# Kernel tuning notes

Measured on AMD Instinct MI355X. Metric: run time of the kernel, lower is better.

## Reference

```python
import jax, jax.numpy as jnp
import numpy as np
from jax import lax

B, T, IN, H = 32, 512, 512, 512
NUM_LAYERS, NUM_DIR = 2, 2


def _lstm_layer(inputs, Wx, Wh, bx, bh, reverse):
    """inputs: [T,B,D]; Wx: [4H,D]; Wh: [4H,H]; bx,bh: [4H]. Returns (hs [T,B,H], hT, cT)."""
    Tn, Bn, _ = inputs.shape
    Hn = Wh.shape[1]
    # Precompute input-to-hidden projections for all timesteps (one big GEMM).
    xg = jnp.einsum('tbd,gd->tbg', inputs, Wx) + bx + bh  # [T,B,4H]
    if reverse:
        xg = xg[::-1]

    def step(carry, xg_t):
        h, c = carry
        g = xg_t + h @ Wh.T  # [B,4H]
        i, f, gg, o = jnp.split(g, 4, axis=-1)  # PyTorch LSTM gate order i,f,g,o
        i = jax.nn.sigmoid(i)
        f = jax.nn.sigmoid(f)
        gg = jnp.tanh(gg)
        o = jax.nn.sigmoid(o)
        c = f * c + i * gg
        h = o * jnp.tanh(c)
        return (h, c), h

    h0 = jnp.zeros((Bn, Hn), dtype=inputs.dtype)
    (hT, cT), hs = lax.scan(step, (h0, h0), xg)
    if reverse:
        hs = hs[::-1]
    return hs, hT, cT


def setup_inputs() -> dict:
    key = jax.random.key(0)
    ks = jax.random.split(key, 20)
    std = 1.0 / np.sqrt(H)
    u = lambda k, shp: jax.random.uniform(k, shp, jnp.float32, -std, std)
    inp = {
        'x': jax.random.normal(ks[0], (B, T, IN), jnp.float32),
        # layer 0: input dim IN, stacked over 2 directions
        'Wx_l0': u(ks[1], (NUM_DIR, 4 * H, IN)),
        'Wh_l0': u(ks[2], (NUM_DIR, 4 * H, H)),
        'bx_l0': u(ks[3], (NUM_DIR, 4 * H)),
        'bh_l0': u(ks[4], (NUM_DIR, 4 * H)),
        # layer 1: input dim 2H (bidirectional concat)
        'Wx_l1': u(ks[5], (NUM_DIR, 4 * H, NUM_DIR * H)),
        'Wh_l1': u(ks[6], (NUM_DIR, 4 * H, H)),
        'bx_l1': u(ks[7], (NUM_DIR, 4 * H)),
        'bh_l1': u(ks[8], (NUM_DIR, 4 * H)),
    }
    return inp


def reference(x, Wx_l0, Wh_l0, bx_l0, bh_l0, Wx_l1, Wh_l1, bx_l1, bh_l1):
    layer_params = [(Wx_l0, Wh_l0, bx_l0, bh_l0), (Wx_l1, Wh_l1, bx_l1, bh_l1)]
    inputs = jnp.transpose(x, (1, 0, 2))  # [T,B,IN] (batch_first -> time-major)
    h_list, c_list = [], []
    for layer in range(NUM_LAYERS):
        Wx, Wh, bx, bh = layer_params[layer]
        dir_outs = []
        for d in range(NUM_DIR):
            hs, hT, cT = _lstm_layer(inputs, Wx[d], Wh[d], bx[d], bh[d], reverse=(d == 1))
            dir_outs.append(hs)
            h_list.append(hT)
            c_list.append(cT)
        inputs = jnp.concatenate(dir_outs, axis=-1)  # [T,B,2H] (dropout=0.0)
    output = jnp.transpose(inputs, (1, 0, 2))  # [B,T,2H]
    h_n = jnp.stack(h_list)  # [num_layers*num_dir, B, H]
    c_n = jnp.stack(c_list)
    return output, h_n, c_n
```

## Files before the change

### kernel.cpp

```cpp
#include <hip/hip_runtime.h>

typedef _Float16 f16;
typedef _Float16 f16x2 __attribute__((ext_vector_type(2)));
typedef _Float16 f16x4 __attribute__((ext_vector_type(4)));
typedef _Float16 f16x8 __attribute__((ext_vector_type(8)));
typedef float f32x4 __attribute__((ext_vector_type(4)));

#define AS1 __attribute__((address_space(1)))
#define AS3 __attribute__((address_space(3)))

static __device__ __forceinline__ float sigf(float x) { return 1.f / (1.f + __expf(-x)); }
static __device__ __forceinline__ float tanh_f(float x) { return 2.f / (1.f + __expf(-2.f * x)) - 1.f; }

__global__ void f2h_kernel(const float* __restrict__ in, f16* __restrict__ out, int n4) {
  const int i = blockIdx.x * blockDim.x + threadIdx.x;
  if (i >= n4) return;
  const float4 v = ((const float4*)in)[i];
  f16x4 o;
  o[0] = (f16)v.x; o[1] = (f16)v.y; o[2] = (f16)v.z; o[3] = (f16)v.w;
  ((f16x4*)out)[i] = o;
}

__global__ void bias_kernel(const float* __restrict__ a, const float* __restrict__ b,
                            float* __restrict__ o, int n) {
  const int i = blockIdx.x * blockDim.x + threadIdx.x;
  if (i < n) o[i] = a[i] + b[i];
}

__global__ __launch_bounds__(256) void gemm_xg(const f16* __restrict__ A,
                                               const f16* __restrict__ Bt,
                                               const float* __restrict__ bias,
                                               f16* __restrict__ outp, int K) {
  __shared__ f16 As[128 * 64];
  __shared__ f16 Bs[128 * 64];
  const int tid = threadIdx.x;
  const int w = tid >> 6, l = tid & 63;
  const int m0 = blockIdx.x << 7, n0 = blockIdx.y << 7;
  const int wm = w >> 1, wn = w & 1;
  f32x4 acc[4][4] = {};

  const int lr8 = l >> 3, lc8 = l & 7;
  const int gcol = (lc8 ^ lr8) << 3;

  for (int k0 = 0; k0 < K; k0 += 64) {
    __syncthreads();
#pragma unroll
    for (int j = 0; j < 4; ++j) {
      const int i = (w << 2) + j;
      const f16* ga = A + (size_t)(m0 + (i << 3) + lr8) * K + (k0 + gcol);
      __builtin_amdgcn_global_load_lds((const AS1 void*)ga, (AS3 void*)(As + (i << 9)), 16, 0, 0);
      const f16* gb = Bt + (size_t)(n0 + (i << 3) + lr8) * K + (k0 + gcol);
      __builtin_amdgcn_global_load_lds((const AS1 void*)gb, (AS3 void*)(Bs + (i << 9)), 16, 0, 0);
    }
    asm volatile("s_waitcnt vmcnt(0)" ::: "memory");
    __syncthreads();

#pragma unroll
    for (int kk = 0; kk < 2; ++kk) {
      const int cb = (kk << 6) + ((l >> 4) << 4);
      f16x8 af[4], bf[4];
#pragma unroll
      for (int a = 0; a < 4; ++a) {
        const int r = (wm << 6) + (a << 4) + (l & 15);
        af[a] = *(const f16x8*)((const char*)As + r * 128 + (cb ^ ((r & 7) << 4)));
      }
#pragma unroll
      for (int b = 0; b < 4; ++b) {
        const int r = (wn << 6) + (b << 4) + (l & 15);
        bf[b] = *(const f16x8*)((const char*)Bs + r * 128 + (cb ^ ((r & 7) << 4)));
      }
#pragma unroll
      for (int a = 0; a < 4; ++a)
#pragma unroll
        for (int b = 0; b < 4; ++b)
          acc[a][b] = __builtin_amdgcn_mfma_f32_16x16x32_f16(af[a], bf[b], acc[a][b], 0, 0, 0);
    }
  }

#pragma unroll
  for (int b = 0; b < 4; ++b) {
    const int col = n0 + (wn << 6) + (b << 4) + (l & 15);
    const float bv = bias[col];
    f16* ob = outp + (size_t)(col >> 11) * (16384ull * 2048) + (col & 2047);
#pragma unroll
    for (int a = 0; a < 4; ++a) {
      const int row0 = m0 + (wm << 6) + (a << 4) + ((l >> 4) << 2);
#pragma unroll
      for (int r = 0; r < 4; ++r)
        ob[(size_t)(row0 + r) * 2048] = (f16)(acc[a][b][r] + bv);
    }
  }
}

__global__ __launch_bounds__(256) void lstm_scan(const f16* __restrict__ Whb,
                                                 const f16* __restrict__ xg,
                                                 f16* __restrict__ hbuf,
                                                 f16* __restrict__ h0_all,
                                                 float* __restrict__ outf,
                                                 float* __restrict__ hn,
                                                 float* __restrict__ cn,
                                                 unsigned* __restrict__ flags,
                                                 const int layer) {
  __shared__ f16 Wh_s[64 * 512];
  __shared__ f16 h_s[32 * 512];
  __shared__ float G_s[4 * 32 * 16];

  const int tid = threadIdx.x;
  const int dir = blockIdx.x >> 5;
  const int s = blockIdx.x & 31;
  const int w = tid >> 6, l = tid & 63;

  {
    const int lr = tid >> 2;
    const int g = lr >> 4, u = lr & 15;
    const char* src = (const char*)(Whb + ((size_t)dir * 2048 + (g << 9) + (s << 4) + u) * 512);
    const int cb0 = (tid & 3) << 8;
#pragma unroll
    for (int c = 0; c < 16; ++c) {
      const int cb = cb0 + (c << 4);
      uint4 v = *(const uint4*)(src + cb);
      *(uint4*)((char*)Wh_s + lr * 1024 + (cb ^ ((lr & 7) << 4))) = v;
    }
  }

  unsigned* cnt = flags + ((layer << 1) + dir) * 32;
  const int bb = tid >> 3;
  const int up = tid & 7;

  float c0 = 0.f, c1 = 0.f;
  __syncthreads();

#pragma unroll 1
  for (int t = 0; t < 512; ++t) {
    const int tau = dir ? (511 - t) : t;
    const f16* xr = xg + (((size_t)dir * 16384 + (size_t)bb * 512 + (size_t)tau) << 11) + (s << 4) + (up << 1);
    const f16x2 xv0 = *(const f16x2*)(xr);
    const f16x2 xv1 = *(const f16x2*)(xr + 512);
    const f16x2 xv2 = *(const f16x2*)(xr + 1024);
    const f16x2 xv3 = *(const f16x2*)(xr + 1536);

    float pi0 = 0.f, pi1 = 0.f, pf0 = 0.f, pf1 = 0.f, pg0 = 0.f, pg1 = 0.f, po0 = 0.f, po1 = 0.f;

    if (t > 0) {
      if (tid == 0) {
        const unsigned tgt = 32u * (unsigned)t;
        int guard = 0;
        while (__hip_atomic_load(cnt, __ATOMIC_ACQUIRE, __HIP_MEMORY_SCOPE_AGENT) < tgt) {
          __builtin_amdgcn_s_sleep(1);
          if (++guard > (1 << 22)) break;
        }
      }
      __syncthreads();
      {
        const unsigned long long* hsrc =
            (const unsigned long long*)(hbuf + ((size_t)((dir << 1) + (t & 1)) << 14));
        const int cbase = up << 7;
#pragma unroll
        for (int c = 0; c < 8; ++c) {
          const int cb = cbase + (c << 4);
          const int qi = (bb << 7) + (cb >> 3);
          unsigned long long v0 =
              __hip_atomic_load((unsigned long long*)(hsrc + qi), __ATOMIC_RELAXED, __HIP_MEMORY_SCOPE_AGENT);
          unsigned long long v1 =
              __hip_atomic_load((unsigned long long*)(hsrc + qi + 1), __ATOMIC_RELAXED, __HIP_MEMORY_SCOPE_AGENT);
          char* d = (char*)h_s + (bb << 10) + (cb ^ ((bb & 7) << 4));
          *(unsigned long long*)d = v0;
          *(unsigned long long*)(d + 8) = v1;
        }
      }
      __syncthreads();

      f32x4 acc0 = {}, acc1 = {};
#pragma unroll
      for (int kk = 0; kk < 16; ++kk) {
        const int cb = (kk << 6) + ((l >> 4) << 4);
        const int ra0 = l & 15;
        const int ra1 = 16 + ra0;
        const int rb = (w << 4) + ra0;
        const f16x8 a0 = *(const f16x8*)((const char*)h_s + (ra0 << 10) + (cb ^ ((ra0 & 7) << 4)));
        const f16x8 a1 = *(const f16x8*)((const char*)h_s + (ra1 << 10) + (cb ^ ((ra1 & 7) << 4)));
        const f16x8 bv = *(const f16x8*)((const char*)Wh_s + (rb << 10) + (cb ^ ((rb & 7) << 4)));
        acc0 = __builtin_amdgcn_mfma_f32_16x16x32_f16(a0, bv, acc0, 0, 0, 0);
        acc1 = __builtin_amdgcn_mfma_f32_16x16x32_f16(a1, bv, acc1, 0, 0, 0);
      }
#pragma unroll
      for (int r = 0; r < 4; ++r) {
        const int dr = ((l >> 4) << 2) + r;
        G_s[((w << 5) + dr) * 16 + (l & 15)] = acc0[r];
        G_s[((w << 5) + 16 + dr) * 16 + (l & 15)] = acc1[r];
      }
      __syncthreads();

      const float* gp = G_s + (bb << 4) + (up << 1);
      const float2 vi = *(const float2*)(gp);
      const float2 vf = *(const float2*)(gp + 512);
      const float2 vg = *(const float2*)(gp + 1024);
      const float2 vo = *(const float2*)(gp + 1536);
      pi0 = vi.x; pi1 = vi.y; pf0 = vf.x; pf1 = vf.y;
      pg0 = vg.x; pg1 = vg.y; po0 = vo.x; po1 = vo.y;
    }

    pi0 += (float)xv0[0]; pi1 += (float)xv0[1];
    pf0 += (float)xv1[0]; pf1 += (float)xv1[1];
    pg0 += (float)xv2[0]; pg1 += (float)xv2[1];
    po0 += (float)xv3[0]; po1 += (float)xv3[1];

    const float i0 = sigf(pi0), i1 = sigf(pi1);
    const float f0 = sigf(pf0), f1 = sigf(pf1);
    const float g0 = tanh_f(pg0), g1 = tanh_f(pg1);
    const float o0 = sigf(po0), o1 = sigf(po1);
    c0 = f0 * c0 + i0 * g0;
    c1 = f1 * c1 + i1 * g1;
    const float h0v = o0 * tanh_f(c0);
    const float h1v = o1 * tanh_f(c1);

    union { f16x2 h2; unsigned u; } pk;
    pk.h2[0] = (f16)h0v; pk.h2[1] = (f16)h1v;

    {
      const size_t e = ((size_t)((dir << 1) + ((t + 1) & 1)) << 14) + ((size_t)bb << 9) + (s << 4) + (up << 1);
      __hip_atomic_store((unsigned*)(hbuf + e), pk.u, __ATOMIC_RELAXED, __HIP_MEMORY_SCOPE_AGENT);
    }
    const size_t orow = (((size_t)bb * 512 + (size_t)tau) << 10) + ((size_t)dir << 9) + (s << 4) + (up << 1);
    if (layer == 0) {
      *(unsigned*)(h0_all + orow) = pk.u;
    } else {
      *(float2*)(outf + orow) = make_float2(h0v, h1v);
    }
    if (t == 511) {
      const size_t nidx = (((size_t)(layer << 1) + (size_t)dir) << 14) + ((size_t)bb << 9) + (s << 4) + (up << 1);
      *(float2*)(hn + nidx) = make_float2(h0v, h1v);
      *(float2*)(cn + nidx) = make_float2(c0, c1);
    }

    asm volatile("s_waitcnt vmcnt(0)" ::: "memory");
    __syncthreads();
    if (tid == 0) atomicAdd(cnt, 1u);
  }
}

extern "C" void kernel_launch(void* const* d_in, const int* in_sizes, int n_in,
                              void* d_out, int out_size, void* d_ws, size_t ws_size,
                              hipStream_t stream) {
  const float* x = (const float*)d_in[0];
  const float* Wx0 = (const float*)d_in[1];
  const float* Wh0 = (const float*)d_in[2];
  const float* bx0 = (const float*)d_in[3];
  const float* bh0 = (const float*)d_in[4];
  const float* Wx1 = (const float*)d_in[5];
  const float* Wh1 = (const float*)d_in[6];
  const float* bx1 = (const float*)d_in[7];
  const float* bh1 = (const float*)d_in[8];

  char* ws = (char*)d_ws;
  size_t off = 0;
  auto alloc = [&](size_t b) { char* p = ws + off; off += (b + 255) & ~(size_t)255; return p; };
  f16* xg = (f16*)alloc(2ull * 16384 * 2048 * 2);
  f16* x_h = (f16*)alloc(16384ull * 512 * 2);
  f16* h0a = (f16*)alloc(16384ull * 1024 * 2);
  f16* Wx0h = (f16*)alloc(2ull * 2048 * 512 * 2);
  f16* Wh0h = (f16*)alloc(2ull * 2048 * 512 * 2);
  f16* Wx1h = (f16*)alloc(2ull * 2048 * 1024 * 2);
  f16* Wh1h = (f16*)alloc(2ull * 2048 * 512 * 2);
  float* bias0 = (float*)alloc(4096 * 4);
  float* bias1 = (float*)alloc(4096 * 4);
  f16* hbuf = (f16*)alloc(2ull * 2 * 32 * 512 * 2);
  unsigned* flags = (unsigned*)alloc(1024);
  if (off > ws_size) return;

  float* outp = (float*)d_out;
  float* hn = outp + 16384ull * 1024;
  float* cn = hn + 4ull * 32 * 512;

  hipMemsetAsync(flags, 0, 1024, stream);

  f2h_kernel<<<dim3(2097152 / 256), 256, 0, stream>>>(x, x_h, 2097152);
  f2h_kernel<<<dim3(524288 / 256), 256, 0, stream>>>(Wx0, Wx0h, 524288);
  f2h_kernel<<<dim3(524288 / 256), 256, 0, stream>>>(Wh0, Wh0h, 524288);
  f2h_kernel<<<dim3(1048576 / 256), 256, 0, stream>>>(Wx1, Wx1h, 1048576);
  f2h_kernel<<<dim3(524288 / 256), 256, 0, stream>>>(Wh1, Wh1h, 524288);
  bias_kernel<<<16, 256, 0, stream>>>(bx0, bh0, bias0, 4096);
  bias_kernel<<<16, 256, 0, stream>>>(bx1, bh1, bias1, 4096);

  dim3 g(128, 32);
  gemm_xg<<<g, 256, 0, stream>>>(x_h, Wx0h, bias0, xg, 512);
  lstm_scan<<<64, 256, 0, stream>>>(Wh0h, xg, hbuf, h0a, nullptr, hn, cn, flags, 0);
  gemm_xg<<<g, 256, 0, stream>>>(h0a, Wx1h, bias1, xg, 1024);
  lstm_scan<<<64, 256, 0, stream>>>(Wh1h, xg, hbuf, nullptr, outp, hn, cn, flags, 1);
}
```

Measured before the change: 5.771 ms.

## Replace shared atomic counter barrier with per-block flags polled by a wavefront

Swaps the single atomicAdd counter used as a cross-block barrier for per-block step flags, each on its own 128-byte line, which a whole wavefront polls in parallel and combines with __all. The flag is now released right after the h store, before the output and final-state writes, so those global writes leave the critical path. It also coalesces the Wh and h loads into shared memory and pads G_s rows to reduce LDS bank conflicts. This removes atomic contention and serialized latency on the recurrent per-timestep barrier, at the cost of more polling traffic.

Result: slower. 6.669 ms (+15.6%).

```diff
diff --git a/kernel.cpp b/kernel.cpp
--- a/kernel.cpp
+++ b/kernel.cpp
@@ -103,27 +103,25 @@
                                                  const int layer) {
   __shared__ f16 Wh_s[64 * 512];
   __shared__ f16 h_s[32 * 512];
-  __shared__ float G_s[4 * 32 * 16];
+  __shared__ float G_s[4 * 32 * 18];
 
   const int tid = threadIdx.x;
   const int dir = blockIdx.x >> 5;
   const int s = blockIdx.x & 31;
   const int w = tid >> 6, l = tid & 63;
 
-  {
-    const int lr = tid >> 2;
+#pragma unroll
+  for (int j = 0; j < 16; ++j) {
+    const int chunk = (j << 8) + tid;
+    const int lr = chunk >> 6;
+    const int cbyte = (chunk & 63) << 4;
     const int g = lr >> 4, u = lr & 15;
-    const char* src = (const char*)(Whb + ((size_t)dir * 2048 + (g << 9) + (s << 4) + u) * 512);
-    const int cb0 = (tid & 3) << 8;
-#pragma unroll
-    for (int c = 0; c < 16; ++c) {
-      const int cb = cb0 + (c << 4);
-      uint4 v = *(const uint4*)(src + cb);
-      *(uint4*)((char*)Wh_s + lr * 1024 + (cb ^ ((lr & 7) << 4))) = v;
-    }
-  }
-
-  unsigned* cnt = flags + ((layer << 1) + dir) * 32;
+    const char* src = (const char*)Whb + (((size_t)dir * 2048 + (g << 9) + (s << 4) + u) << 10) + cbyte;
+    const uint4 v = *(const uint4*)src;
+    *(uint4*)((char*)Wh_s + (lr << 10) + (cbyte ^ ((lr & 7) << 4))) = v;
+  }
+
+  unsigned* fgrp = flags + (((layer << 1) + dir) << 10);
   const int bb = tid >> 3;
   const int up = tid & 7;
 
@@ -142,28 +140,32 @@
     float pi0 = 0.f, pi1 = 0.f, pf0 = 0.f, pf1 = 0.f, pg0 = 0.f, pg1 = 0.f, po0 = 0.f, po1 = 0.f;
 
     if (t > 0) {
-      if (tid == 0) {
-        const unsigned tgt = 32u * (unsigned)t;
+      if (w == 0) {
+        const unsigned tgt = (unsigned)t;
+        const unsigned* myf = fgrp + ((l & 31) << 5);
+        unsigned v = tgt;
         int guard = 0;
-        while (__hip_atomic_load(cnt, __ATOMIC_ACQUIRE, __HIP_MEMORY_SCOPE_AGENT) < tgt) {
+        for (;;) {
+          if (l < 32) v = __hip_atomic_load(myf, __ATOMIC_ACQUIRE, __HIP_MEMORY_SCOPE_AGENT);
+          if (__all((int)(v >= tgt))) break;
           __builtin_amdgcn_s_sleep(1);
           if (++guard > (1 << 22)) break;
         }
       }
       __syncthreads();
       {
-        const unsigned long long* hsrc =
-            (const unsigned long long*)(hbuf + ((size_t)((dir << 1) + (t & 1)) << 14));
-        const int cbase = up << 7;
-#pragma unroll
-        for (int c = 0; c < 8; ++c) {
-          const int cb = cbase + (c << 4);
-          const int qi = (bb << 7) + (cb >> 3);
-          unsigned long long v0 =
-              __hip_atomic_load((unsigned long long*)(hsrc + qi), __ATOMIC_RELAXED, __HIP_MEMORY_SCOPE_AGENT);
-          unsigned long long v1 =
-              __hip_atomic_load((unsigned long long*)(hsrc + qi + 1), __ATOMIC_RELAXED, __HIP_MEMORY_SCOPE_AGENT);
-          char* d = (char*)h_s + (bb << 10) + (cb ^ ((bb & 7) << 4));
+        const f16* hsrc = hbuf + ((size_t)((dir << 1) + (t & 1)) << 14);
+#pragma unroll
+        for (int j = 0; j < 8; ++j) {
+          const int chunk = (j << 8) + tid;
+          const int b = chunk >> 6;
+          const int cbyte = (chunk & 63) << 4;
+          const unsigned long long* sp = (const unsigned long long*)((const char*)hsrc + (b << 10) + cbyte);
+          const unsigned long long v0 =
+              __hip_atomic_load(sp, __ATOMIC_RELAXED, __HIP_MEMORY_SCOPE_AGENT);
+          const unsigned long long v1 =
+              __hip_atomic_load(sp + 1, __ATOMIC_RELAXED, __HIP_MEMORY_SCOPE_AGENT);
+          char* d = (char*)h_s + (b << 10) + (cbyte ^ ((b & 7) << 4));
           *(unsigned long long*)d = v0;
           *(unsigned long long*)(d + 8) = v1;
         }
@@ -186,16 +188,16 @@
 #pragma unroll
       for (int r = 0; r < 4; ++r) {
         const int dr = ((l >> 4) << 2) + r;
-        G_s[((w << 5) + dr) * 16 + (l & 15)] = acc0[r];
-        G_s[((w << 5) + 16 + dr) * 16 + (l & 15)] = acc1[r];
+        G_s[((w << 5) + dr) * 18 + (l & 15)] = acc0[r];
+        G_s[((w << 5) + 16 + dr) * 18 + (l & 15)] = acc1[r];
       }
       __syncthreads();
 
-      const float* gp = G_s + (bb << 4) + (up << 1);
+      const float* gp = G_s + bb * 18 + (up << 1);
       const float2 vi = *(const float2*)(gp);
-      const float2 vf = *(const float2*)(gp + 512);
-      const float2 vg = *(const float2*)(gp + 1024);
-      const float2 vo = *(const float2*)(gp + 1536);
+      const float2 vf = *(const float2*)(gp + 576);
+      const float2 vg = *(const float2*)(gp + 1152);
+      const float2 vo = *(const float2*)(gp + 1728);
       pi0 = vi.x; pi1 = vi.y; pf0 = vf.x; pf1 = vf.y;
       pg0 = vg.x; pg1 = vg.y; po0 = vo.x; po1 = vo.y;
     }
@@ -221,6 +223,11 @@
       const size_t e = ((size_t)((dir << 1) + ((t + 1) & 1)) << 14) + ((size_t)bb << 9) + (s << 4) + (up << 1);
       __hip_atomic_store((unsigned*)(hbuf + e), pk.u, __ATOMIC_RELAXED, __HIP_MEMORY_SCOPE_AGENT);
     }
+    asm volatile("s_waitcnt vmcnt(0)" ::: "memory");
+    __syncthreads();
+    if (tid == 0)
+      __hip_atomic_store(fgrp + (s << 5), (unsigned)(t + 1), __ATOMIC_RELEASE, __HIP_MEMORY_SCOPE_AGENT);
+
     const size_t orow = (((size_t)bb * 512 + (size_t)tau) << 10) + ((size_t)dir << 9) + (s << 4) + (up << 1);
     if (layer == 0) {
       *(unsigned*)(h0_all + orow) = pk.u;
@@ -232,10 +239,6 @@
       *(float2*)(hn + nidx) = make_float2(h0v, h1v);
       *(float2*)(cn + nidx) = make_float2(c0, c1);
     }
-
-    asm volatile("s_waitcnt vmcnt(0)" ::: "memory");
-    __syncthreads();
-    if (tid == 0) atomicAdd(cnt, 1u);
   }
 }
 
@@ -265,14 +268,14 @@
   float* bias0 = (float*)alloc(4096 * 4);
   float* bias1 = (float*)alloc(4096 * 4);
   f16* hbuf = (f16*)alloc(2ull * 2 * 32 * 512 * 2);
-  unsigned* flags = (unsigned*)alloc(1024);
+  unsigned* flags = (unsigned*)alloc(4ull * 1024 * 4);
   if (off > ws_size) return;
 
   float* outp = (float*)d_out;
   float* hn = outp + 16384ull * 1024;
   float* cn = hn + 4ull * 32 * 512;
 
-  hipMemsetAsync(flags, 0, 1024, stream);
+  hipMemsetAsync(flags, 0, 4ull * 1024 * 4, stream);
 
   f2h_kernel<<<dim3(2097152 / 256), 256, 0, stream>>>(x, x_h, 2097152);
   f2h_kernel<<<dim3(524288 / 256), 256, 0, stream>>>(Wx0, Wx0h, 524288);
```
